# Kernel tuning notes

Measured on AMD Instinct MI355X. Metric: run time of the kernel, lower is better.

The kernel has to match this reference:

```python
import jax, jax.numpy as jnp
import numpy as np

B, T, C, H = 2, 2048, 1024, 16
HD = C // H  # 64

def setup_inputs() -> dict:
    key = jax.random.key(0)
    ks = jax.random.split(key, 9)
    s = 0.02
    return {
        "x": jax.random.normal(ks[0], (B, T, C), jnp.float32),
        "Wq": jax.random.normal(ks[1], (C, C), jnp.float32) * s,
        "bq": jax.random.normal(ks[2], (C,), jnp.float32) * s,
        "Wk": jax.random.normal(ks[3], (C, C), jnp.float32) * s,
        "bk": jax.random.normal(ks[4], (C,), jnp.float32) * s,
        "Wv": jax.random.normal(ks[5], (C, C), jnp.float32) * s,
        "bv": jax.random.normal(ks[6], (C,), jnp.float32) * s,
        "Wp": jax.random.normal(ks[7], (C, C), jnp.float32) * s,
        "bp": jax.random.normal(ks[8], (C,), jnp.float32) * s,
    }

def reference(x, Wq, bq, Wk, bk, Wv, bv, Wp, bp):
    Bb, Tt, Cc = x.shape
    hd = Cc // H
    # project and split heads: [B, H, T, hd]
    def heads(W, b):
        return (x @ W.T + b).reshape(Bb, Tt, H, hd).transpose(0, 2, 1, 3)
    q, k, v = heads(Wq, bq), heads(Wk, bk), heads(Wv, bv)
    scale = 1.0 / np.sqrt(hd).astype(np.float32)
    att = jnp.einsum('bhqd,bhkd->bhqk', q, k) * scale
    causal = jnp.tril(jnp.ones((Tt, Tt), bool))
    att = jnp.where(causal[None, None], att, -jnp.inf)
    att = jax.nn.softmax(att, axis=-1)
    y = jnp.einsum('bhqk,bhkd->bhqd', att, v)
    y = y.transpose(0, 2, 1, 3).reshape(Bb, Tt, Cc)
    return y @ Wp.T + bp
```

## Files before the change

kernel.cpp:

```cpp
#include <hip/hip_runtime.h>
#include <hip/hip_bf16.h>

#define Tsz 2048
#define Csz 1024
#define Hn 16

typedef short s8v __attribute__((ext_vector_type(8)));
typedef short s4v __attribute__((ext_vector_type(4)));
typedef float f4v __attribute__((ext_vector_type(4)));

#define QSCALE (0.125f * 1.44269504088896f)

__device__ __forceinline__ unsigned short bfr(float x) {
    return (unsigned short)((__builtin_bit_cast(unsigned, x) + 0x8000u) >> 16);
}
__device__ __forceinline__ unsigned pack2_rn(float a, float b) {
    const unsigned ua = __builtin_bit_cast(unsigned, a) + 0x8000u;
    const unsigned ub = __builtin_bit_cast(unsigned, b) + 0x8000u;
    return (ua >> 16) | (ub & 0xFFFF0000u);
}

__device__ __forceinline__ void gload_lds(const void* g, void* l) {
    __builtin_amdgcn_global_load_lds(
        (const __attribute__((address_space(1))) void*)g,
        (__attribute__((address_space(3))) void*)l, 16, 0, 0);
}

__global__ void cvt6(const float* __restrict__ x, const float* __restrict__ wq,
                     const float* __restrict__ wk, const float* __restrict__ wv,
                     const float* __restrict__ wp,
                     short* __restrict__ xo, short* __restrict__ qo,
                     short* __restrict__ ko, short* __restrict__ vo,
                     short* __restrict__ po) {
    const int bx = blockIdx.x;
    const float* in; short* out; int ib;
    if (bx < 4096) { in = x; out = xo; ib = bx; }
    else {
        const int r = bx - 4096, w = r >> 10;
        ib = r & 1023;
        switch (w) {
            case 0: in = wq; out = qo; break;
            case 1: in = wk; out = ko; break;
            case 2: in = wv; out = vo; break;
            default: in = wp; out = po; break;
        }
    }
    const int i = ib * 1024 + threadIdx.x * 4;
    float4 v = *(const float4*)(in + i);
    int2 o;
    o.x = (int)pack2_rn(v.x, v.y);
    o.y = (int)pack2_rn(v.z, v.w);
    *(int2*)(out + i) = o;
}

__global__ __launch_bounds__(256, 3) void qkv_gemm(
    const short* __restrict__ X,
    const short* __restrict__ Wq, const short* __restrict__ Wk, const short* __restrict__ Wv,
    const float* __restrict__ bq, const float* __restrict__ bk, const float* __restrict__ bv,
    short* __restrict__ Qo, short* __restrict__ Ko, short* __restrict__ Vto)
{
    const int z = blockIdx.z;
    const short* W = (z == 0) ? Wq : (z == 1) ? Wk : Wv;
    const float* bias = (z == 0) ? bq : (z == 1) ? bk : bv;

    __shared__ __align__(16) short Ash[128 * 32];
    __shared__ __align__(16) short Bsh[128 * 32];
    __shared__ __align__(16) short TR[64 * 72];

    const int tid = threadIdx.x, lane = tid & 63, wave = tid >> 6;
    const int ln = lane & 15, hi = lane >> 4;
    const int m0 = blockIdx.x * 128, n0 = blockIdx.y * 128;
    const int wm = (wave >> 1) * 64, wn = (wave & 1) * 64;

    const short* Ag = X + (size_t)(m0 + (tid >> 2)) * Csz + (tid & 3) * 8;
    const short* Bg = W + (size_t)(n0 + (tid >> 2)) * Csz + (tid & 3) * 8;

    f4v acc[4][4];
    #pragma unroll
    for (int mt = 0; mt < 4; mt++)
        #pragma unroll
        for (int nt = 0; nt < 4; nt++)
            #pragma unroll
            for (int i = 0; i < 4; i++) acc[mt][nt][i] = 0.f;

    for (int k0 = 0; k0 < Csz; k0 += 32) {
        __syncthreads();
        gload_lds(Ag + k0, Ash + tid * 8);
        gload_lds(Ag + k0 + (size_t)64 * Csz, Ash + 2048 + tid * 8);
        gload_lds(Bg + k0, Bsh + tid * 8);
        gload_lds(Bg + k0 + (size_t)64 * Csz, Bsh + 2048 + tid * 8);
        __syncthreads();

        s8v af[4], bfr_[4];
        #pragma unroll
        for (int mt = 0; mt < 4; mt++)
            af[mt] = *(const s8v*)(Ash + (wm + mt * 16 + ln) * 32 + hi * 8);
        #pragma unroll
        for (int nt = 0; nt < 4; nt++)
            bfr_[nt] = *(const s8v*)(Bsh + (wn + nt * 16 + ln) * 32 + hi * 8);
        #pragma unroll
        for (int mt = 0; mt < 4; mt++)
            #pragma unroll
            for (int nt = 0; nt < 4; nt++)
                acc[mt][nt] = __builtin_amdgcn_mfma_f32_16x16x32_bf16(af[mt], bfr_[nt], acc[mt][nt], 0, 0, 0);
    }

    if (z == 2) {
        const int b = m0 >> 11, t0 = m0 & 2047;
        float bvv[4];
        #pragma unroll
        for (int nt = 0; nt < 4; nt++) bvv[nt] = bias[n0 + wn + nt * 16 + ln];
        #pragma unroll
        for (int ph = 0; ph < 4; ph++) {
            const int mh = ph >> 1, nh = ph & 1;
            __syncthreads();
            if ((wave >> 1) == mh && (wave & 1) == nh) {
                #pragma unroll
                for (int mt = 0; mt < 4; mt++)
                    #pragma unroll
                    for (int nt = 0; nt < 4; nt++) {
                        int2 pk;
                        pk.x = (int)pack2_rn(acc[mt][nt][0] + bvv[nt], acc[mt][nt][1] + bvv[nt]);
                        pk.y = (int)pack2_rn(acc[mt][nt][2] + bvv[nt], acc[mt][nt][3] + bvv[nt]);
                        *(int2*)(TR + (nt * 16 + ln) * 72 + mt * 16 + hi * 4) = pk;
                    }
            }
            __syncthreads();
            const int chl = tid >> 2, seg = tid & 3;
            const s8v r0 = *(const s8v*)(TR + chl * 72 + seg * 16);
            const s8v r1 = *(const s8v*)(TR + chl * 72 + seg * 16 + 8);
            short* dst = Vto + (size_t)(b * 1024 + n0 + nh * 64 + chl) * Tsz + t0 + mh * 64 + seg * 16;
            *(s8v*)(dst) = r0;
            *(s8v*)(dst + 8) = r1;
        }
        return;
    }

    const float scale = (z == 0) ? QSCALE : 1.0f;
    short* out = (z == 0) ? Qo : Ko;

    #pragma unroll
    for (int nt = 0; nt < 4; nt++) {
        const int col = n0 + wn + nt * 16 + ln;
        const float bvv = bias[col];
        #pragma unroll
        for (int mt = 0; mt < 4; mt++) {
            const int row0 = m0 + wm + mt * 16 + hi * 4;
            #pragma unroll
            for (int i = 0; i < 4; i++)
                out[(size_t)(row0 + i) * Csz + col] = (short)bfr((acc[mt][nt][i] + bvv) * scale);
        }
    }
}

__global__ __launch_bounds__(256, 2) void proj_gemm(
    const short* __restrict__ A, const short* __restrict__ W,
    const float* __restrict__ bias, float* __restrict__ out)
{
    __shared__ __align__(16) short Ash[128 * 32];
    __shared__ __align__(16) short Bsh[64 * 32];

    const int tid = threadIdx.x, lane = tid & 63, wave = tid >> 6;
    const int ln = lane & 15, hi = lane >> 4;
    const int m0 = blockIdx.x * 128, n0 = blockIdx.y * 64;
    const int wm = (wave >> 1) * 64, wn = (wave & 1) * 32;

    const short* Ag = A + (size_t)(m0 + (tid >> 2)) * Csz + (tid & 3) * 8;
    const short* Bg = W + (size_t)(n0 + (tid >> 2)) * Csz + (tid & 3) * 8;

    f4v acc[4][2];
    #pragma unroll
    for (int mt = 0; mt < 4; mt++)
        #pragma unroll
        for (int nt = 0; nt < 2; nt++)
            #pragma unroll
            for (int i = 0; i < 4; i++) acc[mt][nt][i] = 0.f;

    for (int k0 = 0; k0 < Csz; k0 += 32) {
        __syncthreads();
        gload_lds(Ag + k0, Ash + tid * 8);
        gload_lds(Ag + k0 + (size_t)64 * Csz, Ash + 2048 + tid * 8);
        gload_lds(Bg + k0, Bsh + tid * 8);
        __syncthreads();

        s8v af[4], bfr_[2];
        #pragma unroll
        for (int mt = 0; mt < 4; mt++)
            af[mt] = *(const s8v*)(Ash + (wm + mt * 16 + ln) * 32 + hi * 8);
        #pragma unroll
        for (int nt = 0; nt < 2; nt++)
            bfr_[nt] = *(const s8v*)(Bsh + (wn + nt * 16 + ln) * 32 + hi * 8);
        #pragma unroll
        for (int mt = 0; mt < 4; mt++)
            #pragma unroll
            for (int nt = 0; nt < 2; nt++)
                acc[mt][nt] = __builtin_amdgcn_mfma_f32_16x16x32_bf16(af[mt], bfr_[nt], acc[mt][nt], 0, 0, 0);
    }

    #pragma unroll
    for (int nt = 0; nt < 2; nt++) {
        const int col = n0 + wn + nt * 16 + ln;
        const float bvv = bias[col];
        #pragma unroll
        for (int mt = 0; mt < 4; mt++)
            #pragma unroll
            for (int i = 0; i < 4; i++)
                out[(size_t)(m0 + wm + mt * 16 + hi * 4 + i) * Csz + col] = acc[mt][nt][i] + bvv;
    }
}

__global__ __launch_bounds__(256, 4) void attn13(
    const short* __restrict__ Q, const short* __restrict__ Kg,
    const short* __restrict__ Vt, short* __restrict__ Y)
{
    __shared__ __align__(16) short Ksh[64 * 64];
    __shared__ __align__(16) short Vsh[64 * 64];
    __shared__ __align__(16) short Psh[2][4][16 * 72];

    const int tid = threadIdx.x, lane = tid & 63, wave = tid >> 6;
    const int ln = lane & 15, hi = lane >> 4;

    const int n = blockIdx.x;
    const int c = n & 255, j = n >> 8;
    const int bh = (j << 3) | (c >> 5);
    const int t = c & 31;
    const int qt = (j & 1) ? t : 31 - t;

    const size_t base = (size_t)(bh >> 4) * Tsz * Csz + (size_t)(bh & 15) * 64;
    const size_t vtbase = (size_t)bh * 64 * Tsz;
    const int qrel = wave * 16 + ln;

    s8v qf[2];
    #pragma unroll
    for (int kk = 0; kk < 2; kk++)
        qf[kk] = *(const s8v*)(Q + base + (size_t)(qt * 64 + qrel) * Csz + kk * 32 + hi * 8);

    f4v o[4];
    float lsum = 0.f;
    #pragma unroll
    for (int dt = 0; dt < 4; dt++)
        #pragma unroll
        for (int i = 0; i < 4; i++) o[dt][i] = 0.f;

    const int sr = tid >> 3, scs = tid & 7;
    const short* Kp = Kg + base + (size_t)sr * Csz + scs * 8;
    const short* Vp = Vt + vtbase + (size_t)sr * Tsz + scs * 8;
    const int swo = sr * 64 + (scs ^ (sr & 7)) * 8;
    const int nkb = qt + 1;

    int foff[2][4];
    #pragma unroll
    for (int nt = 0; nt < 4; nt++)
        #pragma unroll
        for (int kk = 0; kk < 2; kk++)
            foff[kk][nt] = (nt * 16 + ln) * 64 + (((kk * 4 + hi) ^ (ln & 7)) * 8);

    s8v k0 = *(const s8v*)(Kp);
    s8v k1 = *(const s8v*)(Kp + (size_t)32 * Csz);
    s8v v0 = *(const s8v*)(Vp);
    s8v v1 = *(const s8v*)(Vp + (size_t)32 * Tsz);
    *(s8v*)(&Ksh[swo]) = k0;
    *(s8v*)(&Ksh[swo + 32 * 64]) = k1;
    *(s8v*)(&Vsh[swo]) = v0;
    *(s8v*)(&Vsh[swo + 32 * 64]) = v1;
    __syncthreads();

    s8v vprev[2][4];

    for (int kb = 0; kb < nkb; kb++) {
        const bool more = (kb + 1 < nkb);
        if (more) {
            const size_t ko = (size_t)(kb + 1) * 64;
            k0 = *(const s8v*)(Kp + ko * Csz);
            k1 = *(const s8v*)(Kp + (ko + 32) * Csz);
            v0 = *(const s8v*)(Vp + ko);
            v1 = *(const s8v*)(Vp + ko + (size_t)32 * Tsz);
        }

        s8v kf[2][4];
        #pragma unroll
        for (int nt = 0; nt < 4; nt++)
            #pragma unroll
            for (int kk = 0; kk < 2; kk++)
                kf[kk][nt] = *(const s8v*)(&Ksh[foff[kk][nt]]);

        f4v s[4];
        #pragma unroll
        for (int nt = 0; nt < 4; nt++) {
            #pragma unroll
            for (int i = 0; i < 4; i++) s[nt][i] = 0.f;
            s[nt] = __builtin_amdgcn_mfma_f32_16x16x32_bf16(kf[0][nt], qf[0], s[nt], 0, 0, 0);
            s[nt] = __builtin_amdgcn_mfma_f32_16x16x32_bf16(kf[1][nt], qf[1], s[nt], 0, 0, 0);
        }

        if (kb > 0) {
            const short* Pr = Psh[(kb - 1) & 1][wave];
            const s8v pb0 = *(const s8v*)(Pr + ln * 72 + hi * 8);
            const s8v pb1 = *(const s8v*)(Pr + ln * 72 + 32 + hi * 8);
            #pragma unroll
            for (int dt = 0; dt < 4; dt++) {
                o[dt] = __builtin_amdgcn_mfma_f32_16x16x32_bf16(vprev[0][dt], pb0, o[dt], 0, 0, 0);
                o[dt] = __builtin_amdgcn_mfma_f32_16x16x32_bf16(vprev[1][dt], pb1, o[dt], 0, 0, 0);
            }
        }

        const bool dg = !more;
        short* Pw = Psh[kb & 1][wave];
        #pragma unroll
        for (int nt = 0; nt < 4; nt++) {
            float pv[4];
            #pragma unroll
            for (int i = 0; i < 4; i++) pv[i] = exp2f(s[nt][i]);
            if (dg) {
                const int kr = nt * 16 + hi * 4;
                #pragma unroll
                for (int i = 0; i < 4; i++)
                    if (kr + i > qrel) pv[i] = 0.f;
            }
            lsum += (pv[0] + pv[1]) + (pv[2] + pv[3]);
            int2 w;
            w.x = (int)pack2_rn(pv[0], pv[1]);
            w.y = (int)pack2_rn(pv[2], pv[3]);
            *(int2*)(Pw + ln * 72 + nt * 16 + hi * 4) = w;
        }

        #pragma unroll
        for (int nt = 0; nt < 4; nt++)
            #pragma unroll
            for (int kk = 0; kk < 2; kk++)
                vprev[kk][nt] = *(const s8v*)(&Vsh[foff[kk][nt]]);

        if (more) {
            __syncthreads();
            *(s8v*)(&Ksh[swo]) = k0;
            *(s8v*)(&Ksh[swo + 32 * 64]) = k1;
            *(s8v*)(&Vsh[swo]) = v0;
            *(s8v*)(&Vsh[swo + 32 * 64]) = v1;
            __syncthreads();
        }
    }

    {
        const short* Pr = Psh[(nkb - 1) & 1][wave];
        const s8v pb0 = *(const s8v*)(Pr + ln * 72 + hi * 8);
        const s8v pb1 = *(const s8v*)(Pr + ln * 72 + 32 + hi * 8);
        #pragma unroll
        for (int dt = 0; dt < 4; dt++) {
            o[dt] = __builtin_amdgcn_mfma_f32_16x16x32_bf16(vprev[0][dt], pb0, o[dt], 0, 0, 0);
            o[dt] = __builtin_amdgcn_mfma_f32_16x16x32_bf16(vprev[1][dt], pb1, o[dt], 0, 0, 0);
        }
    }

    float l = lsum;
    l += __shfl_xor(l, 16);
    l += __shfl_xor(l, 32);
    const float inv = 1.0f / l;
    const int qrow = qt * 64 + qrel;
    #pragma unroll
    for (int dt = 0; dt < 4; dt++) {
        int2 w;
        w.x = (int)pack2_rn(o[dt][0] * inv, o[dt][1] * inv);
        w.y = (int)pack2_rn(o[dt][2] * inv, o[dt][3] * inv);
        *(int2*)(Y + base + (size_t)qrow * Csz + dt * 16 + hi * 4) = w;
    }
}

extern "C" void kernel_launch(void* const* d_in, const int* in_sizes, int n_in,
                              void* d_out, int out_size, void* d_ws, size_t ws_size,
                              hipStream_t stream) {
    const float* x  = (const float*)d_in[0];
    const float* Wq = (const float*)d_in[1];
    const float* bq = (const float*)d_in[2];
    const float* Wk = (const float*)d_in[3];
    const float* bk = (const float*)d_in[4];
    const float* Wv = (const float*)d_in[5];
    const float* bv = (const float*)d_in[6];
    const float* Wp = (const float*)d_in[7];
    const float* bp = (const float*)d_in[8];

    char* ws = (char*)d_ws;
    short* Xb  = (short*)(ws);
    short* Wqb = (short*)(ws + (8u  << 20));
    short* Wkb = (short*)(ws + (10u << 20));
    short* Wvb = (short*)(ws + (12u << 20));
    short* Wpb = (short*)(ws + (14u << 20));
    short* Qb  = (short*)(ws + (16u << 20));
    short* Kb  = (short*)(ws + (24u << 20));
    short* Vtb = (short*)(ws + (32u << 20));
    short* Yb  = (short*)(ws + (40u << 20));

    hipLaunchKernelGGL(cvt6, dim3(8192), dim3(256), 0, stream,
                       x, Wq, Wk, Wv, Wp, Xb, Wqb, Wkb, Wvb, Wpb);

    hipLaunchKernelGGL(qkv_gemm, dim3(32, 8, 3), dim3(256), 0, stream,
                       Xb, Wqb, Wkb, Wvb, bq, bk, bv, Qb, Kb, Vtb);

    hipLaunchKernelGGL(attn13, dim3(1024), dim3(256), 0, stream, Qb, Kb, Vtb, Yb);

    hipLaunchKernelGGL(proj_gemm, dim3(32, 16), dim3(256), 0, stream, Yb, Wpb, bp, (float*)d_out);
}
```

Before: 196.6 us.

## Transpose P in registers with permlane swaps instead of LDS round-trip

The attention kernel no longer stages the bf16 probability tile through a per-wave LDS buffer to change its layout for the PV MFMA. It rearranges the packed values with permlane32/permlane16 swap intrinsics and runs the PV MFMA in the same iteration, dropping the one-iteration software pipelining (vprev) and the epilogue. This removes LDS writes and reads plus the P shared buffer, but the PV MFMAs now depend directly on the exp computation in each iteration, which reduces overlap.

```diff
diff --git a/kernel.cpp b/kernel.cpp
--- a/kernel.cpp
+++ b/kernel.cpp
@@ -8,6 +8,8 @@
 typedef short s8v __attribute__((ext_vector_type(8)));
 typedef short s4v __attribute__((ext_vector_type(4)));
 typedef float f4v __attribute__((ext_vector_type(4)));
+typedef int   i4v __attribute__((ext_vector_type(4)));
+typedef unsigned u2v __attribute__((ext_vector_type(2)));
 
 #define QSCALE (0.125f * 1.44269504088896f)
 
@@ -209,13 +211,12 @@
     }
 }
 
-__global__ __launch_bounds__(256, 4) void attn13(
+__global__ __launch_bounds__(256, 4) void attn14(
     const short* __restrict__ Q, const short* __restrict__ Kg,
     const short* __restrict__ Vt, short* __restrict__ Y)
 {
     __shared__ __align__(16) short Ksh[64 * 64];
     __shared__ __align__(16) short Vsh[64 * 64];
-    __shared__ __align__(16) short Psh[2][4][16 * 72];
 
     const int tid = threadIdx.x, lane = tid & 63, wave = tid >> 6;
     const int ln = lane & 15, hi = lane >> 4;
@@ -265,8 +266,6 @@
     *(s8v*)(&Vsh[swo + 32 * 64]) = v1;
     __syncthreads();
 
-    s8v vprev[2][4];
-
     for (int kb = 0; kb < nkb; kb++) {
         const bool more = (kb + 1 < nkb);
         if (more) {
@@ -277,12 +276,14 @@
             v1 = *(const s8v*)(Vp + ko + (size_t)32 * Tsz);
         }
 
-        s8v kf[2][4];
+        s8v kf[2][4], vf[2][4];
         #pragma unroll
         for (int nt = 0; nt < 4; nt++)
             #pragma unroll
-            for (int kk = 0; kk < 2; kk++)
+            for (int kk = 0; kk < 2; kk++) {
                 kf[kk][nt] = *(const s8v*)(&Ksh[foff[kk][nt]]);
+                vf[kk][nt] = *(const s8v*)(&Vsh[foff[kk][nt]]);
+            }
 
         f4v s[4];
         #pragma unroll
@@ -293,19 +294,8 @@
             s[nt] = __builtin_amdgcn_mfma_f32_16x16x32_bf16(kf[1][nt], qf[1], s[nt], 0, 0, 0);
         }
 
-        if (kb > 0) {
-            const short* Pr = Psh[(kb - 1) & 1][wave];
-            const s8v pb0 = *(const s8v*)(Pr + ln * 72 + hi * 8);
-            const s8v pb1 = *(const s8v*)(Pr + ln * 72 + 32 + hi * 8);
-            #pragma unroll
-            for (int dt = 0; dt < 4; dt++) {
-                o[dt] = __builtin_amdgcn_mfma_f32_16x16x32_bf16(vprev[0][dt], pb0, o[dt], 0, 0, 0);
-                o[dt] = __builtin_amdgcn_mfma_f32_16x16x32_bf16(vprev[1][dt], pb1, o[dt], 0, 0, 0);
-            }
-        }
-
         const bool dg = !more;
-        short* Pw = Psh[kb & 1][wave];
+        unsigned pw[4][2];
         #pragma unroll
         for (int nt = 0; nt < 4; nt++) {
             float pv[4];
@@ -318,17 +308,28 @@
                     if (kr + i > qrel) pv[i] = 0.f;
             }
             lsum += (pv[0] + pv[1]) + (pv[2] + pv[3]);
-            int2 w;
-            w.x = (int)pack2_rn(pv[0], pv[1]);
-            w.y = (int)pack2_rn(pv[2], pv[3]);
-            *(int2*)(Pw + ln * 72 + nt * 16 + hi * 4) = w;
-        }
-
-        #pragma unroll
-        for (int nt = 0; nt < 4; nt++)
-            #pragma unroll
-            for (int kk = 0; kk < 2; kk++)
-                vprev[kk][nt] = *(const s8v*)(&Vsh[foff[kk][nt]]);
+            pw[nt][0] = pack2_rn(pv[0], pv[1]);
+            pw[nt][1] = pack2_rn(pv[2], pv[3]);
+        }
+
+        u2v r0a = __builtin_amdgcn_permlane32_swap(pw[0][0], pw[1][0], false, false);
+        u2v r0b = __builtin_amdgcn_permlane16_swap(r0a[0], r0a[1], false, false);
+        u2v r1a = __builtin_amdgcn_permlane32_swap(pw[0][1], pw[1][1], false, false);
+        u2v r1b = __builtin_amdgcn_permlane16_swap(r1a[0], r1a[1], false, false);
+        u2v r2a = __builtin_amdgcn_permlane32_swap(pw[2][0], pw[3][0], false, false);
+        u2v r2b = __builtin_amdgcn_permlane16_swap(r2a[0], r2a[1], false, false);
+        u2v r3a = __builtin_amdgcn_permlane32_swap(pw[2][1], pw[3][1], false, false);
+        u2v r3b = __builtin_amdgcn_permlane16_swap(r3a[0], r3a[1], false, false);
+        i4v p0 = { (int)r0b[0], (int)r1b[0], (int)r0b[1], (int)r1b[1] };
+        i4v p1 = { (int)r2b[0], (int)r3b[0], (int)r2b[1], (int)r3b[1] };
+        const s8v pb0 = __builtin_bit_cast(s8v, p0);
+        const s8v pb1 = __builtin_bit_cast(s8v, p1);
+
+        #pragma unroll
+        for (int dt = 0; dt < 4; dt++) {
+            o[dt] = __builtin_amdgcn_mfma_f32_16x16x32_bf16(vf[0][dt], pb0, o[dt], 0, 0, 0);
+            o[dt] = __builtin_amdgcn_mfma_f32_16x16x32_bf16(vf[1][dt], pb1, o[dt], 0, 0, 0);
+        }
 
         if (more) {
             __syncthreads();
@@ -337,17 +338,6 @@
             *(s8v*)(&Vsh[swo]) = v0;
             *(s8v*)(&Vsh[swo + 32 * 64]) = v1;
             __syncthreads();
-        }
-    }
-
-    {
-        const short* Pr = Psh[(nkb - 1) & 1][wave];
-        const s8v pb0 = *(const s8v*)(Pr + ln * 72 + hi * 8);
-        const s8v pb1 = *(const s8v*)(Pr + ln * 72 + 32 + hi * 8);
-        #pragma unroll
-        for (int dt = 0; dt < 4; dt++) {
-            o[dt] = __builtin_amdgcn_mfma_f32_16x16x32_bf16(vprev[0][dt], pb0, o[dt], 0, 0, 0);
-            o[dt] = __builtin_amdgcn_mfma_f32_16x16x32_bf16(vprev[1][dt], pb1, o[dt], 0, 0, 0);
         }
     }
 
@@ -395,7 +385,7 @@
     hipLaunchKernelGGL(qkv_gemm, dim3(32, 8, 3), dim3(256), 0, stream,
                        Xb, Wqb, Wkb, Wvb, bq, bk, bv, Qb, Kb, Vtb);
 
-    hipLaunchKernelGGL(attn13, dim3(1024), dim3(256), 0, stream, Qb, Kb, Vtb, Yb);
+    hipLaunchKernelGGL(attn14, dim3(1024), dim3(256), 0, stream, Qb, Kb, Vtb, Yb);
 
     hipLaunchKernelGGL(proj_gemm, dim3(32, 16), dim3(256), 0, stream, Yb, Wpb, bp, (float*)d_out);
 }
```

Result: faster. 189.0 us (-3.9%).
